# Optimization experiments

Measured on AMD Instinct MI355X. Metric: run time of the kernel, lower is better.

Reference implementation:

```python
import jax, jax.numpy as jnp
import numpy as np

EPS = 1e-6
T_MAX = 0.999  # occlusion threshold used by compute_paths


def _dot(a, b):
    return jnp.sum(a * b, axis=-1)


def _mirror(p, v, n):
    # Reflect point p across plane through v with unit normal n.
    return p - 2.0 * _dot(p - v, n)[..., None] * n


def image_method(frm, to, mirror_v, mirror_n):
    """frm/to: [...,3]; mirror_v/mirror_n: [...,order,3] -> paths [...,order,3]."""
    order = mirror_v.shape[-2]
    images = []
    cur = frm
    for i in range(order):  # forward pass: successive images of TX
        cur = _mirror(cur, mirror_v[..., i, :], mirror_n[..., i, :])
        images.append(cur)
    paths = [None] * order
    nxt = to
    for i in range(order - 1, -1, -1):  # backward pass: intersect with planes
        img = images[i]
        v = mirror_v[..., i, :]
        n = mirror_n[..., i, :]
        d = nxt - img
        denom = _dot(d, n)
        t = _dot(v - img, n) / jnp.where(jnp.abs(denom) < EPS, EPS, denom)
        nxt = img + t[..., None] * d
        paths[i] = nxt
    return jnp.stack(paths, axis=-2)


def triangles_contain(tv, p):
    """tv: [...,3,3] triangle vertices, p: [...,3] point in same plane -> bool."""
    v0, v1, v2 = tv[..., 0, :], tv[..., 1, :], tv[..., 2, :]
    n0 = jnp.cross(p - v0, v1 - v0)
    n1 = jnp.cross(p - v1, v2 - v1)
    n2 = jnp.cross(p - v2, v0 - v2)
    d01, d12, d20 = _dot(n0, n1), _dot(n1, n2), _dot(n2, n0)
    pos = (d01 >= 0) & (d12 >= 0) & (d20 >= 0)
    neg = (d01 <= 0) & (d12 <= 0) & (d20 <= 0)
    return pos | neg


def same_side_of_mirrors(full_paths, mirror_v, mirror_n):
    """full_paths: [...,order+2,3]; consecutive vertices around each mirror on same side."""
    order = mirror_v.shape[-2]
    prev_v = full_paths[..., :order, :]
    next_v = full_paths[..., 2:, :]
    d_prev = _dot(prev_v - mirror_v, mirror_n)
    d_next = _dot(next_v - mirror_v, mirror_n)
    return d_prev * d_next >= 0


def rays_intersect_triangles(o, d, tv):
    """Moller-Trumbore. o,d: [...,3]; tv: broadcastable [...,3,3] -> (t, hit)."""
    v0, v1, v2 = tv[..., 0, :], tv[..., 1, :], tv[..., 2, :]
    e1 = v1 - v0
    e2 = v2 - v0
    h = jnp.cross(d, e2)
    a = _dot(e1, h)
    inv = 1.0 / jnp.where(jnp.abs(a) < EPS, 1.0, a)
    s = o - v0
    u = _dot(s, h) * inv
    q = jnp.cross(s, e1)
    v = _dot(d, q) * inv
    t = _dot(e2, q) * inv
    hit = (jnp.abs(a) > EPS) & (u >= 0.0) & (v >= 0.0) & (u + v <= 1.0) & (t > EPS)
    return t, hit


def compute_paths(transmitters, receivers, vertices, normals, triangles, path_candidates):
    P = path_candidates.shape[0]
    ntx = transmitters.shape[0]
    nrx = receivers.shape[0]
    all_tv = vertices[triangles]  # [T,3,3]

    frm = jnp.broadcast_to(transmitters[None, :, None, :], (P, ntx, nrx, 3))
    to = jnp.broadcast_to(receivers[None, None, :, :], (P, ntx, nrx, 3))

    pc_tv = all_tv[path_candidates]          # [P,order,3,3]
    mirror_v = pc_tv[..., 0, :]              # [P,order,3]
    mirror_n = normals[path_candidates]      # [P,order,3]
    tvb = pc_tv[:, None, None]               # [P,1,1,order,3,3]
    mvb = mirror_v[:, None, None]            # [P,1,1,order,3]
    mnb = mirror_n[:, None, None]

    paths = image_method(frm, to, mvb, mnb)  # [P,ntx,nrx,order,3]
    mask = jnp.all(triangles_contain(tvb, paths), axis=-1)

    full_paths = jnp.concatenate(
        (frm[..., None, :], paths, to[..., None, :]), axis=-2
    )  # [P,ntx,nrx,order+2,3]
    mask = mask & jnp.all(same_side_of_mirrors(full_paths, mvb, mnb), axis=-1)

    # Occlusion test: each of the order+1 segments vs every mesh triangle.
    ray_o = full_paths[..., :-1, None, :]       # [P,ntx,nrx,order+1,1,3]
    ray_d = jnp.diff(full_paths, axis=-2)[..., None, :]
    t, hit = rays_intersect_triangles(ray_o, ray_d, all_tv)  # [P,ntx,nrx,order+1,T]
    intersect = jnp.any((t < T_MAX) & hit, axis=(-1, -2))
    mask = mask & ~intersect

    # jit-friendly masking (original uses boolean fancy-indexing): zero-out invalid paths.
    return jnp.where(mask[..., None, None], full_paths, 0.0)


def setup_inputs() -> dict:
    key = jax.random.key(0)
    k1, k2, k3, k4 = jax.random.split(key, 4)
    V, T = 100, 128
    transmitters = 5.0 * jax.random.normal(k1, (1, 3), jnp.float32)
    receivers = 5.0 * jax.random.normal(k2, (1, 3), jnp.float32)
    vertices = jax.random.uniform(k3, (V, 3), jnp.float32, -10.0, 10.0)
    triangles = jax.random.randint(k4, (T, 3), 0, V, jnp.int32)
    tv = vertices[triangles]
    n = jnp.cross(tv[:, 1] - tv[:, 0], tv[:, 2] - tv[:, 0])
    normals = n / (jnp.linalg.norm(n, axis=-1, keepdims=True) + 1e-8)
    # generate_all_path_candidates(T, order=2): all ordered pairs (i,j), i != j
    idx = np.arange(T)
    ii, jj = np.meshgrid(idx, idx, indexing="ij")
    m = ii != jj
    path_candidates = jnp.asarray(np.stack([ii[m], jj[m]], axis=-1), jnp.int32)
    return {
        "transmitters": transmitters,
        "receivers": receivers,
        "vertices": vertices,
        "normals": normals,
        "triangles": triangles,
        "path_candidates": path_candidates,
        "order": 2,
    }


def reference(transmitters, receivers, vertices, normals, triangles, path_candidates, order):
    del order  # encoded in path_candidates.shape[-1]
    return compute_paths(transmitters, receivers, vertices, normals, triangles, path_candidates)
```

## Files before the change

### kernel.cpp

```cpp
#include <hip/hip_runtime.h>
#include <hip/hip_bf16.h>

#define EPS_F  1e-6f
#define TMAX_F 0.999f

struct F3 { float x, y, z; };

__device__ __forceinline__ F3 operator-(F3 a, F3 b){ return {a.x-b.x, a.y-b.y, a.z-b.z}; }
__device__ __forceinline__ F3 operator+(F3 a, F3 b){ return {a.x+b.x, a.y+b.y, a.z+b.z}; }
__device__ __forceinline__ F3 operator*(float s, F3 a){ return {s*a.x, s*a.y, s*a.z}; }
__device__ __forceinline__ float dot3(F3 a, F3 b){ return a.x*b.x + a.y*b.y + a.z*b.z; }
__device__ __forceinline__ F3 cross3(F3 a, F3 b){
  return { a.y*b.z - a.z*b.y, a.z*b.x - a.x*b.z, a.x*b.y - a.y*b.x };
}
__device__ __forceinline__ F3 ld3(const float* p){ return {p[0], p[1], p[2]}; }

__device__ __forceinline__ F3 mirror3(F3 p, F3 v, F3 n){
  float d = dot3(p - v, n);
  return p - (2.0f * d) * n;
}

__device__ __forceinline__ F3 plane_pt(F3 img, F3 v, F3 n, F3 nxt){
  F3 d = nxt - img;
  float den = dot3(d, n);
  float sd = (fabsf(den) < EPS_F) ? EPS_F : den;
  float t = dot3(v - img, n) / sd;
  return img + t * d;
}

__device__ __forceinline__ bool tri_contains(const float* tv9, F3 p){
  F3 a = ld3(tv9), b = ld3(tv9+3), c = ld3(tv9+6);
  F3 n0 = cross3(p - a, b - a);
  F3 n1 = cross3(p - b, c - b);
  F3 n2 = cross3(p - c, a - c);
  float d01 = dot3(n0, n1), d12 = dot3(n1, n2), d20 = dot3(n2, n0);
  bool pos = (d01 >= 0.f) & (d12 >= 0.f) & (d20 >= 0.f);
  bool neg = (d01 <= 0.f) & (d12 <= 0.f) & (d20 <= 0.f);
  return pos | neg;
}

__device__ __forceinline__ bool mt_block(F3 o, F3 d, const float* tv9){
  F3 a = ld3(tv9), b = ld3(tv9+3), c = ld3(tv9+6);
  F3 e1 = b - a, e2 = c - a;
  F3 h = cross3(d, e2);
  float det = dot3(e1, h);
  float safep = (fabsf(det) < EPS_F) ? 1.0f : det;
  float inv = 1.0f / safep;
  F3 s = o - a;
  float u = dot3(s, h) * inv;
  F3 q = cross3(s, e1);
  float v = dot3(d, q) * inv;
  float t = dot3(e2, q) * inv;
  bool hit = (fabsf(det) > EPS_F) & (u >= 0.f) & (v >= 0.f) & (u + v <= 1.f) & (t > EPS_F);
  return hit & (t < TMAX_F);
}

__global__ void __launch_bounds__(256)
paths_kernel(const float* __restrict__ txs, const float* __restrict__ rxs,
             const float* __restrict__ vertices, const float* __restrict__ normals,
             const int* __restrict__ triangles, const int* __restrict__ pc,
             int ntx, int nrx, int P, int T, float* __restrict__ out)
{
  extern __shared__ float smem[];
  float* tvS = smem;
  float* nS  = tvS + T * 9;
  float* fpS = nS + T * 3;
  unsigned int* maskS = reinterpret_cast<unsigned int*>(fpS + 64 * 12);
  unsigned int* occlS = maskS + 2;

  const int tid  = threadIdx.x;
  const int lane = tid & 63;
  const int wid  = tid >> 6;

  for (int i = tid; i < T * 3; i += 256) {
    int vi = triangles[i];
    tvS[i*3+0] = vertices[vi*3+0];
    tvS[i*3+1] = vertices[vi*3+1];
    tvS[i*3+2] = vertices[vi*3+2];
    nS[i] = normals[i];
  }
  if (tid < 64) occlS[tid] = 0u;
  __syncthreads();

  const long long total = (long long)P * ntx * nrx;
  const long long cbase = (long long)blockIdx.x * 64;

  if (wid == 0) {
    const long long c = cbase + lane;
    const bool valid = c < total;
    const long long cc = valid ? c : 0;

    const int txrx = ntx * nrx;
    const int p  = (int)(cc / txrx);
    const int r  = (int)(cc % txrx);
    const int tx = r / nrx;
    const int rx = r % nrx;

    const F3 frm = ld3(txs + tx * 3);
    const F3 to  = ld3(rxs + rx * 3);

    const int t0 = pc[p*2 + 0];
    const int t1 = pc[p*2 + 1];

    const F3 v0 = ld3(tvS + t0 * 9);
    const F3 n0 = ld3(nS + t0 * 3);
    const F3 v1 = ld3(tvS + t1 * 9);
    const F3 n1 = ld3(nS + t1 * 3);

    const F3 img0 = mirror3(frm,  v0, n0);
    const F3 img1 = mirror3(img0, v1, n1);
    const F3 p1 = plane_pt(img1, v1, n1, to);
    const F3 p0 = plane_pt(img0, v0, n0, p1);

    bool mask = tri_contains(tvS + t0 * 9, p0) & tri_contains(tvS + t1 * 9, p1);
    float sp0 = dot3(frm - v0, n0) * dot3(p1 - v0, n0);
    float sp1 = dot3(p0  - v1, n1) * dot3(to - v1, n1);
    mask = mask & (sp0 >= 0.f) & (sp1 >= 0.f) & valid;

    float* myfp = fpS + lane * 12;
    myfp[0]=frm.x; myfp[1]=frm.y; myfp[2]=frm.z;
    myfp[3]=p0.x;  myfp[4]=p0.y;  myfp[5]=p0.z;
    myfp[6]=p1.x;  myfp[7]=p1.y;  myfp[8]=p1.z;
    myfp[9]=to.x;  myfp[10]=to.y; myfp[11]=to.z;

    unsigned long long m = __ballot(mask);
    if (lane == 0) {
      maskS[0] = (unsigned int)(m & 0xffffffffu);
      maskS[1] = (unsigned int)(m >> 32);
    }
  }
  __syncthreads();

  {
    unsigned long long alive =
        ((unsigned long long)maskS[1] << 32) | (unsigned long long)maskS[0];
    int item = 0;
    while (alive) {
      const int s = __builtin_ctzll(alive);
      alive &= alive - 1;
      const float* sfp = fpS + s * 12;
      #pragma unroll
      for (int seg = 0; seg < 3; ++seg, ++item) {
        if ((item & 3) != wid) continue;
        F3 o = ld3(sfp + seg * 3);
        F3 e = ld3(sfp + seg * 3 + 3);
        F3 d = e - o;
        bool inter = false;
        for (int tri = lane; tri < T; tri += 64)
          inter |= mt_block(o, d, tvS + tri * 9);
        unsigned long long hb = __ballot(inter);
        if (lane == 0 && hb) occlS[s] = 1u;
      }
    }
  }
  __syncthreads();

  if (tid < 192) {
    const int cand = tid / 3;
    const int quad = tid - cand * 3;
    const long long c = cbase + cand;
    if (c < total) {
      const unsigned int mw = maskS[cand >> 5];
      const bool fin = ((mw >> (cand & 31)) & 1u) && !occlS[cand];
      const float* fp = fpS + cand * 12 + quad * 4;
      float4 val = fin ? make_float4(fp[0], fp[1], fp[2], fp[3])
                       : make_float4(0.f, 0.f, 0.f, 0.f);
      reinterpret_cast<float4*>(out)[c * 3 + quad] = val;
    }
  }
}

extern "C" void kernel_launch(void* const* d_in, const int* in_sizes, int n_in,
                              void* d_out, int out_size, void* d_ws, size_t ws_size,
                              hipStream_t stream) {
  const float* txs       = (const float*)d_in[0];
  const float* rxs       = (const float*)d_in[1];
  const float* vertices  = (const float*)d_in[2];
  const float* normals   = (const float*)d_in[3];
  const int*   triangles = (const int*)d_in[4];
  const int*   pc        = (const int*)d_in[5];

  const int ntx = in_sizes[0] / 3;
  const int nrx = in_sizes[1] / 3;
  const int T   = in_sizes[4] / 3;
  const int P   = in_sizes[5] / 2;

  float* out = (float*)d_out;

  const long long total = (long long)P * ntx * nrx;
  const int grid = (int)((total + 63) / 64);
  const size_t shmem = (size_t)(T * 12 + 64 * 12 + 2 + 64) * sizeof(float);

  paths_kernel<<<grid, 256, shmem, stream>>>(
      txs, rxs, vertices, normals, triangles, pc, ntx, nrx, P, T, out);
}
```

Baseline: 70.27 us.

## Defer shared triangle staging until a block has surviving candidates

Wave 0 now reads the two candidate triangles' vertices and normals straight from global memory, so it no longer depends on the shared-memory copy of the whole mesh. That per-block staging, plus its barrier, now runs only when at least one of the block's 64 candidates passes the geometric mask, so blocks with no surviving candidate skip it. Indexing also moves from 64-bit to 32-bit, with a fast path when there is a single TX/RX pair. The cost is gathered global loads for wave 0, and 32-bit indexing limits the total candidate count.

```diff
diff --git a/kernel.cpp b/kernel.cpp
--- a/kernel.cpp
+++ b/kernel.cpp
@@ -28,8 +28,7 @@
   return img + t * d;
 }
 
-__device__ __forceinline__ bool tri_contains(const float* tv9, F3 p){
-  F3 a = ld3(tv9), b = ld3(tv9+3), c = ld3(tv9+6);
+__device__ __forceinline__ bool tri_contains(F3 a, F3 b, F3 c, F3 p){
   F3 n0 = cross3(p - a, b - a);
   F3 n1 = cross3(p - b, c - b);
   F3 n2 = cross3(p - c, a - c);
@@ -39,8 +38,7 @@
   return pos | neg;
 }
 
-__device__ __forceinline__ bool mt_block(F3 o, F3 d, const float* tv9){
-  F3 a = ld3(tv9), b = ld3(tv9+3), c = ld3(tv9+6);
+__device__ __forceinline__ bool mt_block(F3 o, F3 d, F3 a, F3 b, F3 c){
   F3 e1 = b - a, e2 = c - a;
   F3 h = cross3(d, e2);
   float det = dot3(e1, h);
@@ -59,7 +57,7 @@
 paths_kernel(const float* __restrict__ txs, const float* __restrict__ rxs,
              const float* __restrict__ vertices, const float* __restrict__ normals,
              const int* __restrict__ triangles, const int* __restrict__ pc,
-             int ntx, int nrx, int P, int T, float* __restrict__ out)
+             int ntx, int nrx, int total, int T, float* __restrict__ out)
 {
   extern __shared__ float smem[];
   float* tvS = smem;
@@ -72,47 +70,48 @@
   const int lane = tid & 63;
   const int wid  = tid >> 6;
 
-  for (int i = tid; i < T * 3; i += 256) {
-    int vi = triangles[i];
-    tvS[i*3+0] = vertices[vi*3+0];
-    tvS[i*3+1] = vertices[vi*3+1];
-    tvS[i*3+2] = vertices[vi*3+2];
-    nS[i] = normals[i];
-  }
-  if (tid < 64) occlS[tid] = 0u;
-  __syncthreads();
-
-  const long long total = (long long)P * ntx * nrx;
-  const long long cbase = (long long)blockIdx.x * 64;
+  const int cbase = blockIdx.x * 64;
+
+  if (wid == 1) occlS[lane] = 0u;
 
   if (wid == 0) {
-    const long long c = cbase + lane;
+    const int c = cbase + lane;
     const bool valid = c < total;
-    const long long cc = valid ? c : 0;
+    const int cc = valid ? c : 0;
 
     const int txrx = ntx * nrx;
-    const int p  = (int)(cc / txrx);
-    const int r  = (int)(cc % txrx);
-    const int tx = r / nrx;
-    const int rx = r % nrx;
+    int p, tx, rx;
+    if (txrx == 1) { p = cc; tx = 0; rx = 0; }
+    else {
+      p = cc / txrx;
+      const int r = cc - p * txrx;
+      tx = r / nrx;
+      rx = r - tx * nrx;
+    }
 
     const F3 frm = ld3(txs + tx * 3);
     const F3 to  = ld3(rxs + rx * 3);
 
-    const int t0 = pc[p*2 + 0];
-    const int t1 = pc[p*2 + 1];
-
-    const F3 v0 = ld3(tvS + t0 * 9);
-    const F3 n0 = ld3(nS + t0 * 3);
-    const F3 v1 = ld3(tvS + t1 * 9);
-    const F3 n1 = ld3(nS + t1 * 3);
+    const int2 t01 = reinterpret_cast<const int2*>(pc)[p];
+    const int t0 = t01.x, t1 = t01.y;
+
+    const F3 a0 = ld3(vertices + triangles[t0*3+0]*3);
+    const F3 b0 = ld3(vertices + triangles[t0*3+1]*3);
+    const F3 c0 = ld3(vertices + triangles[t0*3+2]*3);
+    const F3 a1 = ld3(vertices + triangles[t1*3+0]*3);
+    const F3 b1 = ld3(vertices + triangles[t1*3+1]*3);
+    const F3 c1 = ld3(vertices + triangles[t1*3+2]*3);
+    const F3 n0 = ld3(normals + t0 * 3);
+    const F3 n1 = ld3(normals + t1 * 3);
+    const F3 v0 = a0;
+    const F3 v1 = a1;
 
     const F3 img0 = mirror3(frm,  v0, n0);
     const F3 img1 = mirror3(img0, v1, n1);
     const F3 p1 = plane_pt(img1, v1, n1, to);
     const F3 p0 = plane_pt(img0, v0, n0, p1);
 
-    bool mask = tri_contains(tvS + t0 * 9, p0) & tri_contains(tvS + t1 * 9, p1);
+    bool mask = tri_contains(a0, b0, c0, p0) & tri_contains(a1, b1, c1, p1);
     float sp0 = dot3(frm - v0, n0) * dot3(p1 - v0, n0);
     float sp1 = dot3(p0  - v1, n1) * dot3(to - v1, n1);
     mask = mask & (sp0 >= 0.f) & (sp1 >= 0.f) & valid;
@@ -131,9 +130,19 @@
   }
   __syncthreads();
 
-  {
-    unsigned long long alive =
-        ((unsigned long long)maskS[1] << 32) | (unsigned long long)maskS[0];
+  const unsigned int m0 = maskS[0], m1 = maskS[1];
+
+  if (m0 | m1) {
+    for (int i = tid; i < T * 3; i += 256) {
+      int vi = triangles[i];
+      tvS[i*3+0] = vertices[vi*3+0];
+      tvS[i*3+1] = vertices[vi*3+1];
+      tvS[i*3+2] = vertices[vi*3+2];
+      nS[i] = normals[i];
+    }
+    __syncthreads();
+
+    unsigned long long alive = ((unsigned long long)m1 << 32) | m0;
     int item = 0;
     while (alive) {
       const int s = __builtin_ctzll(alive);
@@ -146,26 +155,28 @@
         F3 e = ld3(sfp + seg * 3 + 3);
         F3 d = e - o;
         bool inter = false;
-        for (int tri = lane; tri < T; tri += 64)
-          inter |= mt_block(o, d, tvS + tri * 9);
+        for (int t = lane; t < T; t += 64) {
+          F3 ta = ld3(tvS + t*9), tb = ld3(tvS + t*9 + 3), tc = ld3(tvS + t*9 + 6);
+          inter |= mt_block(o, d, ta, tb, tc);
+        }
         unsigned long long hb = __ballot(inter);
         if (lane == 0 && hb) occlS[s] = 1u;
       }
     }
+    __syncthreads();
   }
-  __syncthreads();
 
   if (tid < 192) {
     const int cand = tid / 3;
     const int quad = tid - cand * 3;
-    const long long c = cbase + cand;
+    const int c = cbase + cand;
     if (c < total) {
-      const unsigned int mw = maskS[cand >> 5];
+      const unsigned int mw = (cand < 32) ? m0 : m1;
       const bool fin = ((mw >> (cand & 31)) & 1u) && !occlS[cand];
       const float* fp = fpS + cand * 12 + quad * 4;
       float4 val = fin ? make_float4(fp[0], fp[1], fp[2], fp[3])
                        : make_float4(0.f, 0.f, 0.f, 0.f);
-      reinterpret_cast<float4*>(out)[c * 3 + quad] = val;
+      reinterpret_cast<float4*>(out)[(size_t)c * 3 + quad] = val;
     }
   }
 }
@@ -192,5 +203,5 @@
   const size_t shmem = (size_t)(T * 12 + 64 * 12 + 2 + 64) * sizeof(float);
 
   paths_kernel<<<grid, 256, shmem, stream>>>(
-      txs, rxs, vertices, normals, triangles, pc, ntx, nrx, P, T, out);
-}
+      txs, rxs, vertices, normals, triangles, pc, ntx, nrx, (int)total, T, out);
+}
```

After: 69.78 us. No clear change (-0.7%).
